# Kernel optimization log

Measured on AMD Instinct MI355X. Metric: run time of the kernel, lower is better.

Reference implementation:

```python
import jax, jax.numpy as jnp
import numpy as np

N = 50000
E_RAND = 800000
E = E_RAND + N  # random edges + self loops
IN_DIM = 128
H = 4
D = 32  # num_hidden
HD = H * D  # 128
N_CLS = 2
NEG_SLOPE = 0.2
BN_EPS = 1e-5


def setup_inputs() -> dict:
    key = jax.random.key(0)
    ks = jax.random.split(key, 32)
    x = jax.random.randint(ks[0], (N,), 0, 200)
    src_r = jax.random.randint(ks[1], (E_RAND,), 0, N)
    dst_r = jax.random.randint(ks[2], (E_RAND,), 0, N)
    loops = jnp.arange(N)
    src = jnp.concatenate([src_r, loops])
    dst = jnp.concatenate([dst_r, loops])
    snorm_n = jax.random.uniform(ks[3], (N, 1), jnp.float32, 0.1, 1.0)
    snorm_e = jax.random.uniform(ks[4], (E, 1), jnp.float32, 0.1, 1.0)

    def nrm(k, shape, fan_in):
        return jax.random.normal(k, shape, jnp.float32) * (1.0 / np.sqrt(fan_in))

    inp = {
        'x': x, 'src': src, 'dst': dst, 'snorm_n': snorm_n, 'snorm_e': snorm_e,
        'embed': nrm(ks[5], (200, IN_DIM), 1.0),
        'W0': nrm(ks[6], (IN_DIM, HD), IN_DIM),
        'al0': nrm(ks[7], (H, D), D), 'ar0': nrm(ks[8], (H, D), D),
        'gamma0': jnp.ones((HD,), jnp.float32), 'beta0': jnp.zeros((HD,), jnp.float32),
        'W1': nrm(ks[9], (HD, HD), HD),
        'al1': nrm(ks[10], (H, D), D), 'ar1': nrm(ks[11], (H, D), D),
        'gamma1': jnp.ones((HD,), jnp.float32), 'beta1': jnp.zeros((HD,), jnp.float32),
        'W2': nrm(ks[12], (HD, HD), HD),
        'al2': nrm(ks[13], (H, D), D), 'ar2': nrm(ks[14], (H, D), D),
        'gamma2': jnp.ones((HD,), jnp.float32), 'beta2': jnp.zeros((HD,), jnp.float32),
        'cls1_w': nrm(ks[15], (HD, HD // 2), HD), 'cls1_b': jnp.zeros((HD // 2,), jnp.float32),
        'cls2_w': nrm(ks[16], (HD // 2, N_CLS), HD // 2), 'cls2_b': jnp.zeros((N_CLS,), jnp.float32),
    }
    return inp


def _gat_conv(h, W, al, ar, src, dst, residual, apply_act):
    # h: [N, F_in]; DGL-style GATConv with edge softmax over destination.
    feat = (h @ W).reshape(N, H, D)                         # [N,H,D]
    el = jnp.sum(feat * al, axis=-1)                        # [N,H]
    er = jnp.sum(feat * ar, axis=-1)                        # [N,H]
    e = jax.nn.leaky_relu(el[src] + er[dst], NEG_SLOPE)     # [E,H]
    m = jax.ops.segment_max(e, dst, num_segments=N)         # per-dst max
    ee = jnp.exp(e - m[dst])
    s = jax.ops.segment_sum(ee, dst, num_segments=N)
    a = ee / s[dst]                                         # edge softmax [E,H]
    msg = feat[src] * a[:, :, None]                         # [E,H,D]
    rst = jax.ops.segment_sum(msg, dst, num_segments=N)     # [N,H,D]
    if residual:
        rst = rst + h.reshape(N, H, D)  # identity residual (dims match)
    if apply_act:
        rst = jax.nn.elu(rst)           # activation inside GATConv (layers > 0)
    return rst.reshape(N, HD)


def _bn(h, gamma, beta):
    mu = jnp.mean(h, axis=0)
    var = jnp.mean((h - mu) ** 2, axis=0)  # biased var, matches torch BN training
    return gamma * (h - mu) * jax.lax.rsqrt(var + BN_EPS) + beta


def reference(x, src, dst, snorm_n, snorm_e, embed,
              W0, al0, ar0, gamma0, beta0,
              W1, al1, ar1, gamma1, beta1,
              W2, al2, ar2, gamma2, beta2,
              cls1_w, cls1_b, cls2_w, cls2_b):
    h = embed[x]  # [N, IN_DIM]
    layers = [
        (W0, al0, ar0, gamma0, beta0, False, False),
        (W1, al1, ar1, gamma1, beta1, True, True),
        (W2, al2, ar2, gamma2, beta2, True, True),
    ]
    for W, al, ar, g, b, res, act in layers:
        h = _gat_conv(h, W, al, ar, src, dst, res, act)
        h = h * snorm_n
        h = _bn(h, g, b)
        h = jax.nn.elu(h)
    h = jax.nn.relu(h @ cls1_w + cls1_b)
    logits = h @ cls2_w + cls2_b  # [N, N_CLS]
    return logits
```

## Files before the change

kernel.cpp:

```cpp
#include <hip/hip_runtime.h>
#include <hip/hip_bf16.h>
#include <hip/hip_fp16.h>
#include <math.h>

constexpr int N_NODES = 50000;
constexpr int N_EDGES = 850000;
constexpr int HDIM = 128;
constexpr int AGG_BLOCKS = N_NODES / 8;
constexpr int BN_BUCKETS = 64;

typedef _Float16 f16x8 __attribute__((ext_vector_type(8)));
typedef float f32x4 __attribute__((ext_vector_type(4)));

constexpr int NB2 = 128;
constexpr int RANGE2 = (N_NODES + NB2 - 1) / NB2;
constexpr int CAP = 8192;
constexpr int CHUNK = 8192;
constexpr int GA = (N_EDGES + CHUNK - 1) / CHUNK;

__global__ void k_partA(const int* __restrict__ src, const int* __restrict__ dst,
                        int* __restrict__ g_cursor, unsigned* __restrict__ bucket) {
    __shared__ int hist[NB2];
    int tid = threadIdx.x;
    int e0 = blockIdx.x * CHUNK;
    int e1 = min(e0 + CHUNK, N_EDGES);
    if (tid < NB2) hist[tid] = 0;
    __syncthreads();
    for (int i = e0 + tid; i < e1; i += 1024) {
        int d = dst[i];
        atomicAdd(&hist[d / RANGE2], 1);
    }
    __syncthreads();
    int base = 0;
    if (tid < NB2) base = atomicAdd(&g_cursor[tid], hist[tid]);
    __syncthreads();
    if (tid < NB2) hist[tid] = base;
    __syncthreads();
    for (int i = e0 + tid; i < e1; i += 1024) {
        int d = dst[i];
        int s = src[i];
        int b = d / RANGE2;
        int p = atomicAdd(&hist[b], 1);
        bucket[b * CAP + p] = (unsigned)s | ((unsigned)(d - b * RANGE2) << 16);
    }
}

__global__ void k_partB(const unsigned* __restrict__ bucket, const int* __restrict__ cnts,
                        int* __restrict__ rowstart, int* __restrict__ esrc) {
    __shared__ int cnt_s[NB2];
    __shared__ int hist[RANGE2];
    __shared__ int lcur[RANGE2];
    __shared__ int wsum[7];
    int b = blockIdx.x, tid = threadIdx.x;
    int lo = b * RANGE2;
    int myCount = cnts[b];
    if (tid < NB2) cnt_s[tid] = cnts[tid];
    __syncthreads();
    for (int off = 1; off < NB2; off <<= 1) {
        int t = (tid < NB2 && tid >= off) ? cnt_s[tid - off] : 0;
        __syncthreads();
        if (tid < NB2) cnt_s[tid] += t;
        __syncthreads();
    }
    int base = cnt_s[b] - myCount;
    for (int j = tid; j < RANGE2; j += 1024) hist[j] = 0;
    __syncthreads();
    const unsigned* my = bucket + (size_t)b * CAP;
    for (int i = tid; i < myCount; i += 1024) atomicAdd(&hist[my[i] >> 16], 1);
    __syncthreads();
    int v = 0;
    if (tid < 448) v = (tid < RANGE2) ? hist[tid] : 0;
    int inc = v;
    int lane = tid & 63;
#pragma unroll
    for (int off = 1; off < 64; off <<= 1) {
        int t = __shfl_up(inc, off, 64);
        if (lane >= off) inc += t;
    }
    if (tid < 448 && lane == 63) wsum[tid >> 6] = inc;
    __syncthreads();
    if (tid < RANGE2) {
        int woff = 0;
        for (int w = 0; w < (tid >> 6); w++) woff += wsum[w];
        int excl = woff + inc - v;
        lcur[tid] = excl;
        int node = lo + tid;
        if (node < N_NODES) rowstart[node] = base + excl;
    }
    if (b == 0 && tid == 0) rowstart[N_NODES] = N_EDGES;
    __syncthreads();
    for (int i = tid; i < myCount; i += 1024) {
        unsigned p = my[i];
        int pos = atomicAdd(&lcur[p >> 16], 1);
        esrc[base + pos] = (int)(p & 0xFFFFu);
    }
}

__global__ void k_wpack(const float* __restrict__ W0, const float* __restrict__ W1,
                        const float* __restrict__ W2, __half* __restrict__ wpk,
                        float* __restrict__ bn_part, int* __restrict__ g_cursor) {
    int gid = blockIdx.x * 256 + threadIdx.x;
    {
        int z0 = gid * 8;
        if (z0 < 3 * BN_BUCKETS * 256) {
            float4 z = make_float4(0.f, 0.f, 0.f, 0.f);
            *reinterpret_cast<float4*>(&bn_part[z0]) = z;
            *reinterpret_cast<float4*>(&bn_part[z0 + 4]) = z;
        }
        if (gid < NB2) g_cursor[gid] = 0;
    }
    if (gid >= 3 * 2048) return;
    int L = gid >> 11;
    int rem = gid & 2047;
    int ct = rem >> 8;
    int kc = (rem >> 6) & 3;
    int l = rem & 63;
    const float* W = (L == 0) ? W0 : ((L == 1) ? W1 : W2);
    int c = ct * 16 + (l & 15);
    int k0 = kc * 32 + (l >> 4) * 8;
    __half tmp[8];
#pragma unroll
    for (int j = 0; j < 8; j++) tmp[j] = __float2half(W[(k0 + j) * HDIM + c]);
    *reinterpret_cast<float4*>(&wpk[((size_t)L << 14) + ((size_t)(ct * 4 + kc) * 64 + l) * 8]) =
        *reinterpret_cast<float4*>(tmp);
}

__global__ void k_gemm5(const __half* __restrict__ h, const int* __restrict__ xidx,
                        const float* __restrict__ embed, const f16x8* __restrict__ wB,
                        __half* __restrict__ feat_h, const float* __restrict__ bnsc,
                        const float* __restrict__ bnsh, const float* __restrict__ al,
                        const float* __restrict__ ar, float* __restrict__ el,
                        float* __restrict__ er, int mode) {
    __shared__ __half sf[4][16][136];
    int tid = threadIdx.x;
    int w = tid >> 6, lane = tid & 63;
    int r = lane & 15, kg = lane >> 4;
    int wbase = blockIdx.x * 64 + w * 16;
    int n = wbase + r;
    bool ok = n < N_NODES;

    f16x8 aF[4];
#pragma unroll
    for (int kc = 0; kc < 4; kc++)
#pragma unroll
        for (int j = 0; j < 8; j++) aF[kc][j] = (_Float16)0.f;
    if (ok) {
        if (mode == 0) {
            int xi = xidx[n];
            const float* ep = embed + (size_t)xi * HDIM;
#pragma unroll
            for (int kc = 0; kc < 4; kc++) {
                int c0 = kc * 32 + kg * 8;
                float4 e0 = *reinterpret_cast<const float4*>(ep + c0);
                float4 e1 = *reinterpret_cast<const float4*>(ep + c0 + 4);
                aF[kc][0] = (_Float16)e0.x; aF[kc][1] = (_Float16)e0.y;
                aF[kc][2] = (_Float16)e0.z; aF[kc][3] = (_Float16)e0.w;
                aF[kc][4] = (_Float16)e1.x; aF[kc][5] = (_Float16)e1.y;
                aF[kc][6] = (_Float16)e1.z; aF[kc][7] = (_Float16)e1.w;
            }
        } else {
            const __half* hp = h + (size_t)n * HDIM;
#pragma unroll
            for (int kc = 0; kc < 4; kc++) {
                int c0 = kc * 32 + kg * 8;
                float4 raw = *reinterpret_cast<const float4*>(hp + c0);
                const __half2* u = reinterpret_cast<const __half2*>(&raw);
                float4 sc0 = *reinterpret_cast<const float4*>(&bnsc[c0]);
                float4 sc1 = *reinterpret_cast<const float4*>(&bnsc[c0 + 4]);
                float4 sh0 = *reinterpret_cast<const float4*>(&bnsh[c0]);
                float4 sh1 = *reinterpret_cast<const float4*>(&bnsh[c0 + 4]);
                float scv[8] = {sc0.x, sc0.y, sc0.z, sc0.w, sc1.x, sc1.y, sc1.z, sc1.w};
                float shv[8] = {sh0.x, sh0.y, sh0.z, sh0.w, sh1.x, sh1.y, sh1.z, sh1.w};
                float vv[8];
#pragma unroll
                for (int t = 0; t < 4; t++) {
                    vv[2 * t] = __half2float(__low2half(u[t]));
                    vv[2 * t + 1] = __half2float(__high2half(u[t]));
                }
#pragma unroll
                for (int j = 0; j < 8; j++) {
                    float t = vv[j] * scv[j] + shv[j];
                    t = (t > 0.f) ? t : expm1f(t);
                    aF[kc][j] = (_Float16)t;
                }
            }
        }
    }

    f32x4 acc[8] = {};
#pragma unroll
    for (int kc = 0; kc < 4; kc++) {
#pragma unroll
        for (int ct = 0; ct < 8; ct++) {
            f16x8 bF = wB[(ct * 4 + kc) * 64 + lane];
            acc[ct] = __builtin_amdgcn_mfma_f32_16x16x32_f16(aF[kc], bF, acc[ct], 0, 0, 0);
        }
    }

#pragma unroll
    for (int ct = 0; ct < 8; ct++)
#pragma unroll
        for (int reg = 0; reg < 4; reg++)
            sf[w][kg * 4 + reg][ct * 16 + r] = __float2half(acc[ct][reg]);
    __syncthreads();
#pragma unroll
    for (int q = 0; q < 4; q++) {
        int row = q * 4 + kg;
        int n2 = wbase + row;
        if (n2 < N_NODES) {
            float4 v = *reinterpret_cast<const float4*>(&sf[w][row][r * 8]);
            *reinterpret_cast<float4*>(&feat_h[(size_t)n2 * HDIM + r * 8]) = v;
        }
    }

    float alq[8], arq[8];
#pragma unroll
    for (int ct = 0; ct < 8; ct++) {
        alq[ct] = al[ct * 16 + r];
        arq[ct] = ar[ct * 16 + r];
    }
#pragma unroll
    for (int hd = 0; hd < 4; hd++) {
        float pl[4], pr[4];
#pragma unroll
        for (int reg = 0; reg < 4; reg++) {
            pl[reg] = acc[2 * hd][reg] * alq[2 * hd] + acc[2 * hd + 1][reg] * alq[2 * hd + 1];
            pr[reg] = acc[2 * hd][reg] * arq[2 * hd] + acc[2 * hd + 1][reg] * arq[2 * hd + 1];
        }
#pragma unroll
        for (int off = 1; off < 16; off <<= 1)
#pragma unroll
            for (int reg = 0; reg < 4; reg++) {
                pl[reg] += __shfl_xor(pl[reg], off, 64);
                pr[reg] += __shfl_xor(pr[reg], off, 64);
            }
        if (r == 0) {
#pragma unroll
            for (int reg = 0; reg < 4; reg++) {
                int n2 = wbase + kg * 4 + reg;
                if (n2 < N_NODES) {
                    el[n2 * 4 + hd] = pl[reg];
                    er[n2 * 4 + hd] = pr[reg];
                }
            }
        }
    }
}

__global__ void k_agg9(const __half* __restrict__ feat_h, const float* __restrict__ el,
                       const float* __restrict__ er, const int* __restrict__ rowstart,
                       const int* __restrict__ esrc, const float* __restrict__ snorm_n,
                       __half* __restrict__ h, const float* __restrict__ bnsc,
                       const float* __restrict__ bnsh, float* __restrict__ bn_part,
                       int layer) {
    __shared__ __align__(16) int2 lds[4][2][2][32][4];
    int tid = threadIdx.x;
    int wave = tid >> 6, lane = tid & 63;
    int h2 = lane >> 5, hl = lane & 31;
    int dp = hl & 15, epair = hl >> 4, head = dp >> 2;
    int n = blockIdx.x * 8 + wave * 2 + h2;
    int e0 = rowstart[n];
    int deg = rowstart[n + 1] - e0;
    int dmax = max(deg, __shfl_xor(deg, 32, 64));
    float4 er4 = *(const float4*)&er[n * 4];
    const float4* fp = reinterpret_cast<const float4*>(feat_h);
    float s = 0.f;
    float a[8] = {};
    int nch = (dmax + 31) >> 5;

    int idx0 = e0 + min(hl, deg - 1);
    int sidx_p = esrc[idx0];
    float4 el_p = *(const float4*)&el[sidx_p * 4];
    bool val_p = hl < deg;

    for (int c = 0; c < nch; c++) {
        float w0 = 0.f, w1 = 0.f, w2 = 0.f, w3 = 0.f;
        int sv = sidx_p;
        if (val_p) {
            float ex = el_p.x + er4.x, ey = el_p.y + er4.y;
            float ez = el_p.z + er4.z, ew = el_p.w + er4.w;
            ex = fmaxf(ex, 0.f) + 0.2f * fminf(ex, 0.f);
            ey = fmaxf(ey, 0.f) + 0.2f * fminf(ey, 0.f);
            ez = fmaxf(ez, 0.f) + 0.2f * fminf(ez, 0.f);
            ew = fmaxf(ew, 0.f) + 0.2f * fminf(ew, 0.f);
            w0 = __expf(ex); w1 = __expf(ey); w2 = __expf(ez); w3 = __expf(ew);
        }
        int4* wp = reinterpret_cast<int4*>(&lds[wave][h2][c & 1][hl][0]);
        wp[0] = make_int4(sv, __float_as_int(w0), sv, __float_as_int(w1));
        wp[1] = make_int4(sv, __float_as_int(w2), sv, __float_as_int(w3));
        if (c + 1 < nch) {
            int slot = (c + 1) * 32 + hl;
            int idx = e0 + min(slot, deg - 1);
            sidx_p = esrc[idx];
            el_p = *(const float4*)&el[sidx_p * 4];
            val_p = slot < deg;
        }
        int cnt = min(32, dmax - c * 32);
        int iters = (cnt + 1) >> 1;
#pragma unroll 2
        for (int j = 0; j < iters; j++) {
            int2 rec = lds[wave][h2][c & 1][j * 2 + epair][head];
            float w = __int_as_float(rec.y);
            float4 fv = fp[(size_t)rec.x * 16 + dp];
            __half2 p0 = *(__half2*)&fv.x, p1 = *(__half2*)&fv.y;
            __half2 p2 = *(__half2*)&fv.z, p3 = *(__half2*)&fv.w;
            a[0] = fmaf(__half2float(__low2half(p0)), w, a[0]);
            a[1] = fmaf(__half2float(__high2half(p0)), w, a[1]);
            a[2] = fmaf(__half2float(__low2half(p1)), w, a[2]);
            a[3] = fmaf(__half2float(__high2half(p1)), w, a[3]);
            a[4] = fmaf(__half2float(__low2half(p2)), w, a[4]);
            a[5] = fmaf(__half2float(__high2half(p2)), w, a[5]);
            a[6] = fmaf(__half2float(__low2half(p3)), w, a[6]);
            a[7] = fmaf(__half2float(__high2half(p3)), w, a[7]);
            s += w;
        }
    }
#pragma unroll
    for (int k = 0; k < 8; k++) a[k] += __shfl_xor(a[k], 16, 64);
    s += __shfl_xor(s, 16, 64);
    float r[8] = {};
    if (epair == 0) {
        float inv = 1.f / s;
        int d0 = dp * 8;
#pragma unroll
        for (int k = 0; k < 8; k++) r[k] = a[k] * inv;
        if (layer > 0) {
            float4 hraw = *reinterpret_cast<const float4*>(&h[(size_t)n * HDIM + d0]);
            __half2 q0 = *(__half2*)&hraw.x, q1 = *(__half2*)&hraw.y;
            __half2 q2 = *(__half2*)&hraw.z, q3 = *(__half2*)&hraw.w;
            float hv[8] = {__half2float(__low2half(q0)), __half2float(__high2half(q0)),
                           __half2float(__low2half(q1)), __half2float(__high2half(q1)),
                           __half2float(__low2half(q2)), __half2float(__high2half(q2)),
                           __half2float(__low2half(q3)), __half2float(__high2half(q3))};
            float4 sc0 = *reinterpret_cast<const float4*>(&bnsc[d0]);
            float4 sc1 = *reinterpret_cast<const float4*>(&bnsc[d0 + 4]);
            float4 sh0 = *reinterpret_cast<const float4*>(&bnsh[d0]);
            float4 sh1 = *reinterpret_cast<const float4*>(&bnsh[d0 + 4]);
            float scv[8] = {sc0.x, sc0.y, sc0.z, sc0.w, sc1.x, sc1.y, sc1.z, sc1.w};
            float shv[8] = {sh0.x, sh0.y, sh0.z, sh0.w, sh1.x, sh1.y, sh1.z, sh1.w};
#pragma unroll
            for (int k = 0; k < 8; k++) {
                float t = hv[k] * scv[k] + shv[k];
                t = (t > 0.f) ? t : expm1f(t);
                r[k] += t;
                r[k] = (r[k] > 0.f) ? r[k] : expm1f(r[k]);
            }
        }
        float sn = snorm_n[n];
#pragma unroll
        for (int k = 0; k < 8; k++) r[k] *= sn;
        float4 outv;
        *(__half2*)&outv.x = __floats2half2_rn(r[0], r[1]);
        *(__half2*)&outv.y = __floats2half2_rn(r[2], r[3]);
        *(__half2*)&outv.z = __floats2half2_rn(r[4], r[5]);
        *(__half2*)&outv.w = __floats2half2_rn(r[6], r[7]);
        *reinterpret_cast<float4*>(&h[(size_t)n * HDIM + d0]) = outv;
    }

    float* bsum = reinterpret_cast<float*>(lds);
    __syncthreads();
    if (epair == 0) {
        int n8 = wave * 2 + h2;
        int cbase = n8 * 128 + dp * 8;
#pragma unroll
        for (int k = 0; k < 8; k++) {
            bsum[cbase + k] = r[k];
            bsum[1024 + cbase + k] = r[k] * r[k];
        }
    }
    __syncthreads();
    {
        int c = tid & 127, which = tid >> 7;
        float v = 0.f;
#pragma unroll
        for (int n8 = 0; n8 < 8; n8++) v += bsum[which * 1024 + n8 * 128 + c];
        atomicAdd(&bn_part[(blockIdx.x & (BN_BUCKETS - 1)) * 256 + which * 128 + c], v);
    }
}

__global__ void k_bnfin(const float* __restrict__ bn_part, const float* __restrict__ gamma,
                        const float* __restrict__ beta, float* __restrict__ scale,
                        float* __restrict__ shift) {
    __shared__ float red[256];
    int tid = threadIdx.x;
    int c = tid & 127, which = tid >> 7;
    float t = 0.f;
    for (int b = 0; b < BN_BUCKETS; b++) t += bn_part[b * 256 + which * 128 + c];
    red[tid] = t;
    __syncthreads();
    if (tid < 128) {
        float mu = red[tid] * (1.f / N_NODES);
        float var = red[128 + tid] * (1.f / N_NODES) - mu * mu;
        float sc = gamma[tid] * rsqrtf(var + 1e-5f);
        scale[tid] = sc;
        shift[tid] = beta[tid] - mu * sc;
    }
}

__global__ void k_classifier(const __half* __restrict__ h, const float* __restrict__ W1,
                             const float* __restrict__ b1, const float* __restrict__ W2,
                             const float* __restrict__ b2, const float* __restrict__ bnsc,
                             const float* __restrict__ bnsh, float* __restrict__ out) {
    __shared__ float hs[16][128];
    int tid = threadIdx.x;
    int nbase = blockIdx.x * 16;
    for (int i = tid; i < 16 * 128; i += 256) {
        int r = i >> 7, c = i & 127;
        int n = nbase + r;
        float v = 0.f;
        if (n < N_NODES) {
            v = __half2float(h[(size_t)n * HDIM + c]) * bnsc[c] + bnsh[c];
            v = (v > 0.f) ? v : expm1f(v);
        }
        hs[r][c] = v;
    }
    __syncthreads();
    int j = tid & 63;
    int g = tid >> 6;
    float bj = b1[j];
    float acc[4] = {bj, bj, bj, bj};
    for (int k = 0; k < 128; k++) {
        float w = W1[k * 64 + j];
#pragma unroll
        for (int i = 0; i < 4; i++) acc[i] += hs[g * 4 + i][k] * w;
    }
    float w20 = W2[j * 2], w21 = W2[j * 2 + 1];
    float res[8];
#pragma unroll
    for (int i = 0; i < 4; i++) {
        float hid = fmaxf(acc[i], 0.f);
        res[2 * i] = hid * w20;
        res[2 * i + 1] = hid * w21;
    }
#pragma unroll
    for (int off = 1; off < 64; off <<= 1)
#pragma unroll
        for (int i = 0; i < 8; i++) res[i] += __shfl_xor(res[i], off, 64);
    if (j < 8) {
        int n = nbase + g * 4 + (j >> 1);
        if (n < N_NODES) out[n * 2 + (j & 1)] = res[j] + b2[j & 1];
    }
}

extern "C" void kernel_launch(void* const* d_in, const int* in_sizes, int n_in,
                              void* d_out, int out_size, void* d_ws, size_t ws_size,
                              hipStream_t stream) {
    const int* x = (const int*)d_in[0];
    const int* src = (const int*)d_in[1];
    const int* dst = (const int*)d_in[2];
    const float* snorm_n = (const float*)d_in[3];
    const float* embed = (const float*)d_in[5];
    const float* Ws[3] = {(const float*)d_in[6], (const float*)d_in[11], (const float*)d_in[16]};
    const float* als[3] = {(const float*)d_in[7], (const float*)d_in[12], (const float*)d_in[17]};
    const float* ars[3] = {(const float*)d_in[8], (const float*)d_in[13], (const float*)d_in[18]};
    const float* gms[3] = {(const float*)d_in[9], (const float*)d_in[14], (const float*)d_in[19]};
    const float* bts[3] = {(const float*)d_in[10], (const float*)d_in[15], (const float*)d_in[20]};
    const float* cls1_w = (const float*)d_in[21];
    const float* cls1_b = (const float*)d_in[22];
    const float* cls2_w = (const float*)d_in[23];
    const float* cls2_b = (const float*)d_in[24];
    float* out = (float*)d_out;

    char* ws = (char*)d_ws;
    size_t off = 0;
    auto alloc = [&](size_t bytes) {
        void* p = ws + off;
        off = (off + bytes + 255) & ~(size_t)255;
        return p;
    };
    __half* h = (__half*)alloc((size_t)N_NODES * HDIM * 2);
    __half* feat_h = (__half*)alloc((size_t)N_NODES * HDIM * 2);
    float* el = (float*)alloc((size_t)N_NODES * 4 * 4);
    float* er = (float*)alloc((size_t)N_NODES * 4 * 4);
    int* rowstart = (int*)alloc((size_t)(N_NODES + 1) * 4);
    int* esrc = (int*)alloc((size_t)N_EDGES * 4);
    int* g_cursor = (int*)alloc((size_t)NB2 * 4);
    float* bn_part = (float*)alloc((size_t)3 * BN_BUCKETS * 256 * 4);
    float* bn_scale = (float*)alloc(128 * 4);
    float* bn_shift = (float*)alloc(128 * 4);
    __half* wpkh = (__half*)alloc((size_t)3 * 16384 * 2);
    unsigned* g_bucket = (unsigned*)feat_h;
    (void)ws_size; (void)in_sizes; (void)n_in; (void)out_size;

    k_wpack<<<(3 * 2048 + 255) / 256, 256, 0, stream>>>(Ws[0], Ws[1], Ws[2], wpkh,
                                                        bn_part, g_cursor);
    k_partA<<<GA, 1024, 0, stream>>>(src, dst, g_cursor, g_bucket);
    k_partB<<<NB2, 1024, 0, stream>>>(g_bucket, g_cursor, rowstart, esrc);

    for (int L = 0; L < 3; L++) {
        const f16x8* wB = reinterpret_cast<const f16x8*>(wpkh + ((size_t)L << 14));
        k_gemm5<<<(N_NODES + 63) / 64, 256, 0, stream>>>(h, x, embed, wB,
                                                         feat_h, bn_scale, bn_shift,
                                                         als[L], ars[L], el, er, L == 0 ? 0 : 1);
        k_agg9<<<AGG_BLOCKS, 256, 0, stream>>>(feat_h, el, er, rowstart, esrc,
                                               snorm_n, h, bn_scale, bn_shift,
                                               bn_part + (size_t)L * BN_BUCKETS * 256, L);
        k_bnfin<<<1, 256, 0, stream>>>(bn_part + (size_t)L * BN_BUCKETS * 256,
                                       gms[L], bts[L], bn_scale, bn_shift);
    }

    k_classifier<<<(N_NODES + 15) / 16, 256, 0, stream>>>(h, cls1_w, cls1_b, cls2_w, cls2_b,
                                                          bn_scale, bn_shift, out);
}
```

Before: 341.2 us.

## Fold BN finalize into consumer kernels and reduce atomic bucket count

Removes the single-block k_bnfin launch after each layer. Every block of the next gemm, agg and classifier kernel now reduces the BN partial sums itself and computes scale and shift into shared memory. The bucket count for BN atomics drops from 64 to 16, so each block has less to redundantly reduce, at the cost of more atomic contention. Three tiny serialized launches go away, but every block now does extra global reads and syncs up front.

```diff
diff --git a/kernel.cpp b/kernel.cpp
--- a/kernel.cpp
+++ b/kernel.cpp
@@ -7,7 +7,7 @@
 constexpr int N_EDGES = 850000;
 constexpr int HDIM = 128;
 constexpr int AGG_BLOCKS = N_NODES / 8;
-constexpr int BN_BUCKETS = 64;
+constexpr int BN_BUCKETS = 16;
 
 typedef _Float16 f16x8 __attribute__((ext_vector_type(8)));
 typedef float f32x4 __attribute__((ext_vector_type(4)));
@@ -125,14 +125,33 @@
         *reinterpret_cast<float4*>(tmp);
 }
 
-__global__ void k_gemm5(const __half* __restrict__ h, const int* __restrict__ xidx,
+__global__ void k_gemm6(const __half* __restrict__ h, const int* __restrict__ xidx,
                         const float* __restrict__ embed, const f16x8* __restrict__ wB,
-                        __half* __restrict__ feat_h, const float* __restrict__ bnsc,
-                        const float* __restrict__ bnsh, const float* __restrict__ al,
-                        const float* __restrict__ ar, float* __restrict__ el,
-                        float* __restrict__ er, int mode) {
+                        __half* __restrict__ feat_h, const float* __restrict__ bn_prev,
+                        const float* __restrict__ gamma, const float* __restrict__ beta,
+                        const float* __restrict__ al, const float* __restrict__ ar,
+                        float* __restrict__ el, float* __restrict__ er, int mode) {
     __shared__ __half sf[4][16][136];
+    __shared__ __align__(16) float s_sc[128];
+    __shared__ __align__(16) float s_sh[128];
     int tid = threadIdx.x;
+    if (mode != 0) {
+        float* red = reinterpret_cast<float*>(sf);
+        int c = tid & 127, which = tid >> 7;
+        float t = 0.f;
+#pragma unroll
+        for (int b = 0; b < BN_BUCKETS; b++) t += bn_prev[b * 256 + which * 128 + c];
+        red[tid] = t;
+        __syncthreads();
+        if (tid < 128) {
+            float mu = red[tid] * (1.f / N_NODES);
+            float var = red[128 + tid] * (1.f / N_NODES) - mu * mu;
+            float sc = gamma[tid] * rsqrtf(var + 1e-5f);
+            s_sc[tid] = sc;
+            s_sh[tid] = beta[tid] - mu * sc;
+        }
+        __syncthreads();
+    }
     int w = tid >> 6, lane = tid & 63;
     int r = lane & 15, kg = lane >> 4;
     int wbase = blockIdx.x * 64 + w * 16;
@@ -165,10 +184,10 @@
                 int c0 = kc * 32 + kg * 8;
                 float4 raw = *reinterpret_cast<const float4*>(hp + c0);
                 const __half2* u = reinterpret_cast<const __half2*>(&raw);
-                float4 sc0 = *reinterpret_cast<const float4*>(&bnsc[c0]);
-                float4 sc1 = *reinterpret_cast<const float4*>(&bnsc[c0 + 4]);
-                float4 sh0 = *reinterpret_cast<const float4*>(&bnsh[c0]);
-                float4 sh1 = *reinterpret_cast<const float4*>(&bnsh[c0 + 4]);
+                float4 sc0 = *reinterpret_cast<const float4*>(&s_sc[c0]);
+                float4 sc1 = *reinterpret_cast<const float4*>(&s_sc[c0 + 4]);
+                float4 sh0 = *reinterpret_cast<const float4*>(&s_sh[c0]);
+                float4 sh1 = *reinterpret_cast<const float4*>(&s_sh[c0 + 4]);
                 float scv[8] = {sc0.x, sc0.y, sc0.z, sc0.w, sc1.x, sc1.y, sc1.z, sc1.w};
                 float shv[8] = {sh0.x, sh0.y, sh0.z, sh0.w, sh1.x, sh1.y, sh1.z, sh1.w};
                 float vv[8];
@@ -186,6 +205,7 @@
             }
         }
     }
+    if (mode != 0) __syncthreads();
 
     f32x4 acc[8] = {};
 #pragma unroll
@@ -247,14 +267,33 @@
     }
 }
 
-__global__ void k_agg9(const __half* __restrict__ feat_h, const float* __restrict__ el,
-                       const float* __restrict__ er, const int* __restrict__ rowstart,
-                       const int* __restrict__ esrc, const float* __restrict__ snorm_n,
-                       __half* __restrict__ h, const float* __restrict__ bnsc,
-                       const float* __restrict__ bnsh, float* __restrict__ bn_part,
-                       int layer) {
+__global__ void k_agg10(const __half* __restrict__ feat_h, const float* __restrict__ el,
+                        const float* __restrict__ er, const int* __restrict__ rowstart,
+                        const int* __restrict__ esrc, const float* __restrict__ snorm_n,
+                        __half* __restrict__ h, const float* __restrict__ bn_prev,
+                        const float* __restrict__ gamma, const float* __restrict__ beta,
+                        float* __restrict__ bn_cur, int layer) {
     __shared__ __align__(16) int2 lds[4][2][2][32][4];
+    __shared__ __align__(16) float s_sc[128];
+    __shared__ __align__(16) float s_sh[128];
     int tid = threadIdx.x;
+    if (layer > 0) {
+        float* red = reinterpret_cast<float*>(lds);
+        int c = tid & 127, which = tid >> 7;
+        float t = 0.f;
+#pragma unroll
+        for (int b = 0; b < BN_BUCKETS; b++) t += bn_prev[b * 256 + which * 128 + c];
+        red[tid] = t;
+        __syncthreads();
+        if (tid < 128) {
+            float mu = red[tid] * (1.f / N_NODES);
+            float var = red[128 + tid] * (1.f / N_NODES) - mu * mu;
+            float sc = gamma[tid] * rsqrtf(var + 1e-5f);
+            s_sc[tid] = sc;
+            s_sh[tid] = beta[tid] - mu * sc;
+        }
+        __syncthreads();
+    }
     int wave = tid >> 6, lane = tid & 63;
     int h2 = lane >> 5, hl = lane & 31;
     int dp = hl & 15, epair = hl >> 4, head = dp >> 2;
@@ -332,10 +371,10 @@
                            __half2float(__low2half(q1)), __half2float(__high2half(q1)),
                            __half2float(__low2half(q2)), __half2float(__high2half(q2)),
                            __half2float(__low2half(q3)), __half2float(__high2half(q3))};
-            float4 sc0 = *reinterpret_cast<const float4*>(&bnsc[d0]);
-            float4 sc1 = *reinterpret_cast<const float4*>(&bnsc[d0 + 4]);
-            float4 sh0 = *reinterpret_cast<const float4*>(&bnsh[d0]);
-            float4 sh1 = *reinterpret_cast<const float4*>(&bnsh[d0 + 4]);
+            float4 sc0 = *reinterpret_cast<const float4*>(&s_sc[d0]);
+            float4 sc1 = *reinterpret_cast<const float4*>(&s_sc[d0 + 4]);
+            float4 sh0 = *reinterpret_cast<const float4*>(&s_sh[d0]);
+            float4 sh1 = *reinterpret_cast<const float4*>(&s_sh[d0 + 4]);
             float scv[8] = {sc0.x, sc0.y, sc0.z, sc0.w, sc1.x, sc1.y, sc1.z, sc1.w};
             float shv[8] = {sh0.x, sh0.y, sh0.z, sh0.w, sh1.x, sh1.y, sh1.z, sh1.w};
 #pragma unroll
@@ -374,42 +413,43 @@
         float v = 0.f;
 #pragma unroll
         for (int n8 = 0; n8 < 8; n8++) v += bsum[which * 1024 + n8 * 128 + c];
-        atomicAdd(&bn_part[(blockIdx.x & (BN_BUCKETS - 1)) * 256 + which * 128 + c], v);
-    }
-}
-
-__global__ void k_bnfin(const float* __restrict__ bn_part, const float* __restrict__ gamma,
-                        const float* __restrict__ beta, float* __restrict__ scale,
-                        float* __restrict__ shift) {
-    __shared__ float red[256];
-    int tid = threadIdx.x;
-    int c = tid & 127, which = tid >> 7;
-    float t = 0.f;
-    for (int b = 0; b < BN_BUCKETS; b++) t += bn_part[b * 256 + which * 128 + c];
-    red[tid] = t;
-    __syncthreads();
-    if (tid < 128) {
-        float mu = red[tid] * (1.f / N_NODES);
-        float var = red[128 + tid] * (1.f / N_NODES) - mu * mu;
-        float sc = gamma[tid] * rsqrtf(var + 1e-5f);
-        scale[tid] = sc;
-        shift[tid] = beta[tid] - mu * sc;
+        atomicAdd(&bn_cur[(blockIdx.x & (BN_BUCKETS - 1)) * 256 + which * 128 + c], v);
     }
 }
 
 __global__ void k_classifier(const __half* __restrict__ h, const float* __restrict__ W1,
                              const float* __restrict__ b1, const float* __restrict__ W2,
-                             const float* __restrict__ b2, const float* __restrict__ bnsc,
-                             const float* __restrict__ bnsh, float* __restrict__ out) {
+                             const float* __restrict__ b2, const float* __restrict__ bn_prev,
+                             const float* __restrict__ gamma, const float* __restrict__ beta,
+                             float* __restrict__ out) {
     __shared__ float hs[16][128];
+    __shared__ __align__(16) float s_sc[128];
+    __shared__ __align__(16) float s_sh[128];
     int tid = threadIdx.x;
+    {
+        float* red = &hs[0][0];
+        int c = tid & 127, which = tid >> 7;
+        float t = 0.f;
+#pragma unroll
+        for (int b = 0; b < BN_BUCKETS; b++) t += bn_prev[b * 256 + which * 128 + c];
+        red[tid] = t;
+        __syncthreads();
+        if (tid < 128) {
+            float mu = red[tid] * (1.f / N_NODES);
+            float var = red[128 + tid] * (1.f / N_NODES) - mu * mu;
+            float sc = gamma[tid] * rsqrtf(var + 1e-5f);
+            s_sc[tid] = sc;
+            s_sh[tid] = beta[tid] - mu * sc;
+        }
+        __syncthreads();
+    }
     int nbase = blockIdx.x * 16;
     for (int i = tid; i < 16 * 128; i += 256) {
         int r = i >> 7, c = i & 127;
         int n = nbase + r;
         float v = 0.f;
         if (n < N_NODES) {
-            v = __half2float(h[(size_t)n * HDIM + c]) * bnsc[c] + bnsh[c];
+            v = __half2float(h[(size_t)n * HDIM + c]) * s_sc[c] + s_sh[c];
             v = (v > 0.f) ? v : expm1f(v);
         }
         hs[r][c] = v;
@@ -476,8 +516,6 @@
     int* esrc = (int*)alloc((size_t)N_EDGES * 4);
     int* g_cursor = (int*)alloc((size_t)NB2 * 4);
     float* bn_part = (float*)alloc((size_t)3 * BN_BUCKETS * 256 * 4);
-    float* bn_scale = (float*)alloc(128 * 4);
-    float* bn_shift = (float*)alloc(128 * 4);
     __half* wpkh = (__half*)alloc((size_t)3 * 16384 * 2);
     unsigned* g_bucket = (unsigned*)feat_h;
     (void)ws_size; (void)in_sizes; (void)n_in; (void)out_size;
@@ -489,16 +527,18 @@
 
     for (int L = 0; L < 3; L++) {
         const f16x8* wB = reinterpret_cast<const f16x8*>(wpkh + ((size_t)L << 14));
-        k_gemm5<<<(N_NODES + 63) / 64, 256, 0, stream>>>(h, x, embed, wB,
-                                                         feat_h, bn_scale, bn_shift,
+        const float* bn_prev = bn_part + (size_t)(L == 0 ? 0 : L - 1) * BN_BUCKETS * 256;
+        float* bn_cur = bn_part + (size_t)L * BN_BUCKETS * 256;
+        int gprev = (L == 0) ? 0 : L - 1;
+        k_gemm6<<<(N_NODES + 63) / 64, 256, 0, stream>>>(h, x, embed, wB, feat_h,
+                                                         bn_prev, gms[gprev], bts[gprev],
                                                          als[L], ars[L], el, er, L == 0 ? 0 : 1);
-        k_agg9<<<AGG_BLOCKS, 256, 0, stream>>>(feat_h, el, er, rowstart, esrc,
-                                               snorm_n, h, bn_scale, bn_shift,
-                                               bn_part + (size_t)L * BN_BUCKETS * 256, L);
-        k_bnfin<<<1, 256, 0, stream>>>(bn_part + (size_t)L * BN_BUCKETS * 256,
-                                       gms[L], bts[L], bn_scale, bn_shift);
+        k_agg10<<<AGG_BLOCKS, 256, 0, stream>>>(feat_h, el, er, rowstart, esrc,
+                                                snorm_n, h, bn_prev, gms[gprev], bts[gprev],
+                                                bn_cur, L);
     }
 
     k_classifier<<<(N_NODES + 15) / 16, 256, 0, stream>>>(h, cls1_w, cls1_b, cls2_w, cls2_b,
-                                                          bn_scale, bn_shift, out);
-}
+                                                          bn_part + (size_t)2 * BN_BUCKETS * 256,
+                                                          gms[2], bts[2], out);
+}
```

Result: no change. 339.5 us (-0.5%).
